# Performance work log

Hardware: AMD Instinct MI355X
Metric: run time of the kernel (lower is better)

Reference implementation:

```python
import jax, jax.numpy as jnp
import numpy as np

ALPHA = 4.0          # init alpha
THRESH = 0.693       # validity threshold (~ln 2) from the torch code
K = 8                # instances per class (labels are grouped in blocks of K)
N = 2048
D = 512
NUM_CLASSES = N // K


def setup_inputs() -> dict:
    key = jax.random.key(0)
    inputs = jax.random.normal(key, (N, D), dtype=jnp.float32)
    # grouped labels: [0]*K, [1]*K, ... (required by the original masked_select/resize logic)
    targets = jnp.repeat(jnp.arange(NUM_CLASSES, dtype=jnp.int32), K)
    return {"inputs": inputs, "targets": targets}


def reference(inputs, targets):
    n = inputs.shape[0]
    # x = alpha * L2-normalize(inputs)
    x = ALPHA * inputs / jnp.linalg.norm(inputs, axis=1, keepdims=True)
    # squared euclidean distance matrix [n, n]
    sq = jnp.sum(x * x, axis=1, keepdims=True)
    dist = sq + sq.T - 2.0 * (x @ x.T)

    eye = jnp.eye(n, dtype=bool)
    same = targets[:, None] == targets[None, :]
    pos_mask = same & ~eye            # positives (excluding self)
    neg_mask = ~same                  # negatives

    m = K - 1                         # positives per row
    n_neg = n - K                     # negatives per row
    # stable argsort puts True (0 after ~) positions first, preserving row-major order
    pos_idx = jnp.argsort(~pos_mask, axis=1)[:, :m]
    neg_idx = jnp.argsort(~neg_mask, axis=1)[:, :n_neg]
    pos_dist = jnp.take_along_axis(dist, pos_idx, axis=1)   # [n, m]
    neg_dist = jnp.take_along_axis(dist, neg_idx, axis=1)   # [n, n_neg]

    # triplet_mat[i, j, k] = log(exp(pos[i,k] - neg[i,j]) + 1)
    trip = jnp.log1p(jnp.exp(pos_dist[:, None, :] - neg_dist[:, :, None]))  # [n, n_neg, m]
    valid = trip > THRESH
    cnt = jnp.sum(valid, axis=(1, 2))                        # valid triplets per row
    row_sum = jnp.sum(jnp.where(valid, trip, 0.0), axis=(1, 2))
    row_mean = jnp.where(cnt > 0, row_sum / jnp.maximum(cnt, 1), 0.0)
    total = jnp.sum(cnt)
    loss = jnp.where(total > 0, jnp.sum(row_mean) / total, 0.0)

    accuracy = jnp.mean((cnt == 0).astype(jnp.float32))
    pos_d = jnp.mean(pos_dist)
    neg_d = jnp.mean(neg_dist)
    return loss, accuracy, pos_d, neg_d
```

## Files before the change

### kernel.cpp

```cpp
#include <hip/hip_runtime.h>
#include <hip/hip_bf16.h>
#include <math.h>

#define N 2048
#define D 512
#define KC 8
#define M (KC - 1)
#define NNEG (N - KC)
#define ALPHA 4.0f
#define THRESH 0.693f
#define LN2F 0.6931471805599453f
#define INV_LN2F 1.4426950408889634f
#define C2 (THRESH * INV_LN2F)

typedef unsigned short ushort_t;
using frag_ab = __attribute__((ext_vector_type(8))) short;
using frag_cd = __attribute__((ext_vector_type(4))) float;

__device__ __forceinline__ void gload16(const ushort_t* g, ushort_t* l) {
    __builtin_amdgcn_global_load_lds((const __attribute__((address_space(1))) unsigned int*)g,
                                     (__attribute__((address_space(3))) unsigned int*)l, 16, 0, 0);
}

__global__ __launch_bounds__(128) void normalize_kernel(const float* __restrict__ in,
                                                        ushort_t* __restrict__ xb,
                                                        float* __restrict__ sq) {
    int row = blockIdx.x;
    int tid = threadIdx.x;
    const float* r = in + (size_t)row * D;
    float p = 0.f;
    for (int d = tid; d < D; d += 128) { float v = r[d]; p += v * v; }
    __shared__ float red[128];
    red[tid] = p; __syncthreads();
    for (int s = 64; s > 0; s >>= 1) { if (tid < s) red[tid] += red[tid + s]; __syncthreads(); }
    float scale = ALPHA / sqrtf(red[0]);
    __syncthreads();
    float q = 0.f;
    for (int d = tid; d < D; d += 128) {
        float v = r[d] * scale;
        q += v * v;
        __hip_bfloat16 h = __float2bfloat16(v);
        xb[(size_t)row * D + d] = *(ushort_t*)&h;
    }
    red[tid] = q; __syncthreads();
    for (int s = 64; s > 0; s >>= 1) { if (tid < s) red[tid] += red[tid + s]; __syncthreads(); }
    if (tid == 0) sq[row] = red[0];
}

#define TM 64
#define TN 64
#define TK 64
#define NT (D / TK)

__global__ __launch_bounds__(256) void gemm_dist_mfma(const ushort_t* __restrict__ xb,
                                                      const float* __restrict__ sq,
                                                      float* __restrict__ dist) {
    __shared__ ushort_t As[2 * TM * TK];
    __shared__ ushort_t Bs[2 * TN * TK];
    int tid  = threadIdx.x;
    int lane = tid & 63;
    int w    = tid >> 6;
    int wm   = w >> 1, wn = w & 1;
    int quad = lane >> 4, l16 = lane & 15;
    int bi = blockIdx.y, bj = blockIdx.x;

    frag_cd acc[2][2];
    #pragma unroll
    for (int i = 0; i < 2; ++i)
        #pragma unroll
        for (int j = 0; j < 2; ++j)
            acc[i][j] = (frag_cd){0.f, 0.f, 0.f, 0.f};

    int c0 = tid, c1 = tid + 256;
    int r0 = c0 >> 3, sl0 = c0 & 7;
    int r1 = c1 >> 3, sl1 = c1 & 7;
    int g0 = (sl0 ^ (r0 & 7)) * 8;
    int g1 = (sl1 ^ (r1 & 7)) * 8;
    const ushort_t* gA0 = xb + (size_t)(bi * TM + r0) * D + g0;
    const ushort_t* gA1 = xb + (size_t)(bi * TM + r1) * D + g1;
    const ushort_t* gB0 = xb + (size_t)(bj * TN + r0) * D + g0;
    const ushort_t* gB1 = xb + (size_t)(bj * TN + r1) * D + g1;
    ushort_t* lA0 = As + c0 * 8;
    ushort_t* lA1 = As + c1 * 8;
    ushort_t* lB0 = Bs + c0 * 8;
    ushort_t* lB1 = Bs + c1 * 8;

    int xm = l16 & 7;
    int aoff[2][2], boff[2][2];
    #pragma unroll
    for (int i = 0; i < 2; ++i)
        #pragma unroll
        for (int kk = 0; kk < 2; ++kk) {
            aoff[i][kk] = (wm * 32 + i * 16 + l16) * TK + ((kk * 4 + quad) ^ xm) * 8;
            boff[i][kk] = (wn * 32 + i * 16 + l16) * TK + ((kk * 4 + quad) ^ xm) * 8;
        }

    gload16(gA0, lA0); gload16(gA1, lA1); gload16(gB0, lB0); gload16(gB1, lB1);
    int cur = 0;
    for (int t = 0; t < NT; ++t) {
        __syncthreads();
        if (t + 1 < NT) {
            int k0 = (t + 1) * TK;
            int bo = (cur ^ 1) * (TM * TK);
            gload16(gA0 + k0, lA0 + bo);
            gload16(gA1 + k0, lA1 + bo);
            gload16(gB0 + k0, lB0 + bo);
            gload16(gB1 + k0, lB1 + bo);
        }
        const ushort_t* Ab = As + cur * (TM * TK);
        const ushort_t* Bb = Bs + cur * (TN * TK);
        frag_ab a[2][2], b[2][2];
        #pragma unroll
        for (int i = 0; i < 2; ++i)
            #pragma unroll
            for (int kk = 0; kk < 2; ++kk) {
                a[i][kk] = *(const frag_ab*)(Ab + aoff[i][kk]);
                b[i][kk] = *(const frag_ab*)(Bb + boff[i][kk]);
            }
        #pragma unroll
        for (int kk = 0; kk < 2; ++kk)
            #pragma unroll
            for (int i = 0; i < 2; ++i)
                #pragma unroll
                for (int j = 0; j < 2; ++j)
                    acc[i][j] = __builtin_amdgcn_mfma_f32_16x16x32_bf16(a[i][kk], b[j][kk], acc[i][j], 0, 0, 0);
        cur ^= 1;
    }

    int row_base = bi * TM + wm * 32 + quad * 4;
    int col_base = bj * TN + wn * 32 + l16;
    #pragma unroll
    for (int j = 0; j < 2; ++j) {
        int col = col_base + j * 16;
        float sjv = sq[col];
        #pragma unroll
        for (int i = 0; i < 2; ++i) {
            int row = row_base + i * 16;
            #pragma unroll
            for (int r = 0; r < 4; ++r) {
                dist[(size_t)(row + r) * N + col] = sq[row + r] + sjv - 2.f * acc[i][j][r];
            }
        }
    }
}

__global__ __launch_bounds__(256) void triplet_kernel(const float* __restrict__ dist,
                                                      float4* __restrict__ rowres) {
    int i = blockIdx.x;
    int tid = threadIdx.x;
    int cs = (i >> 3) << 3;
    const float* drow = dist + (size_t)i * N;

    __shared__ float pos[M];
    if (tid == 0) {
        int c = 0;
        for (int j = cs; j < cs + KC; ++j)
            if (j != i) pos[c++] = drow[j];
    }
    __syncthreads();
    float p[M], ep[M];
    #pragma unroll
    for (int k = 0; k < M; ++k) { p[k] = pos[k]; ep[k] = __expf(p[k]); }

    float s2 = 0.f, nsum = 0.f;
    unsigned cnt = 0;
    for (int j = tid; j < N; j += 256) {
        if (j >= cs && j < cs + KC) continue;
        float neg = drow[j];
        nsum += neg;
        float en = __expf(-neg);
        #pragma unroll
        for (int k = 0; k < M; ++k) {
            float e = ep[k] * en;
            float l = __log2f(1.f + e);
            if (l > C2) { cnt++; s2 += l; }
        }
    }

    __shared__ float rs[256];
    __shared__ float rn[256];
    __shared__ unsigned rc[256];
    rs[tid] = s2; rn[tid] = nsum; rc[tid] = cnt;
    __syncthreads();
    for (int st = 128; st > 0; st >>= 1) {
        if (tid < st) { rs[tid] += rs[tid + st]; rn[tid] += rn[tid + st]; rc[tid] += rc[tid + st]; }
        __syncthreads();
    }
    if (tid == 0) {
        float psum = 0.f;
        #pragma unroll
        for (int k = 0; k < M; ++k) psum += p[k];
        rowres[i] = make_float4(rs[0], (float)rc[0], psum, rn[0]);
    }
}

__global__ __launch_bounds__(256) void final_reduce_kernel(const float4* __restrict__ rowres,
                                                           float* __restrict__ out) {
    int tid = threadIdx.x;
    double srm = 0.0, ps = 0.0, ns = 0.0;
    unsigned long long tot = 0; unsigned zr = 0;
    for (int i = tid; i < N; i += 256) {
        float4 r = rowres[i];
        unsigned c = (unsigned)r.y;
        if (c > 0) {
            float row_mean = r.x * LN2F / (float)c;
            srm += (double)row_mean;
            tot += c;
        } else {
            zr++;
        }
        ps += (double)r.z;
        ns += (double)r.w;
    }
    __shared__ double d0[256], d1[256], d2[256];
    __shared__ unsigned long long dt[256];
    __shared__ unsigned dz[256];
    d0[tid] = srm; d1[tid] = ps; d2[tid] = ns; dt[tid] = tot; dz[tid] = zr;
    __syncthreads();
    for (int st = 128; st > 0; st >>= 1) {
        if (tid < st) {
            d0[tid] += d0[tid + st]; d1[tid] += d1[tid + st]; d2[tid] += d2[tid + st];
            dt[tid] += dt[tid + st]; dz[tid] += dz[tid + st];
        }
        __syncthreads();
    }
    if (tid == 0) {
        unsigned long long total = dt[0];
        out[0] = (total > 0) ? (float)(d0[0] / (double)total) : 0.f;
        out[1] = (float)((double)dz[0] / (double)N);
        out[2] = (float)(d1[0] / (double)((size_t)N * M));
        out[3] = (float)(d2[0] / (double)((size_t)N * NNEG));
    }
}

extern "C" void kernel_launch(void* const* d_in, const int* in_sizes, int n_in,
                              void* d_out, int out_size, void* d_ws, size_t ws_size,
                              hipStream_t stream) {
    const float* inputs = (const float*)d_in[0];
    float* out = (float*)d_out;
    char* ws = (char*)d_ws;

    const size_t off_xb   = 0;
    const size_t off_sq   = off_xb + (size_t)N * D * sizeof(ushort_t);
    const size_t off_dist = off_sq + (size_t)N * sizeof(float) + 4096;
    const size_t off_row  = off_dist + (size_t)N * N * sizeof(float);
    const size_t needed   = off_row + (size_t)N * sizeof(float4);
    if (ws_size < needed) return;

    ushort_t* xb     = (ushort_t*)(ws + off_xb);
    float*    sq     = (float*)(ws + off_sq);
    float*    dist   = (float*)(ws + off_dist);
    float4*   rowres = (float4*)(ws + off_row);

    normalize_kernel<<<N, 128, 0, stream>>>(inputs, xb, sq);
    gemm_dist_mfma<<<dim3(N / TN, N / TM), 256, 0, stream>>>(xb, sq, dist);
    triplet_kernel<<<N, 256, 0, stream>>>(dist, rowres);
    final_reduce_kernel<<<1, 256, 0, stream>>>(rowres, out);
}
```

Baseline: 90.33 us.

## Fuse final reduction into triplet kernel and vectorize negative loads

Merges the single-block final reduction into the triplet kernel using a last-block-done atomic counter, which the GEMM kernel resets, saving one kernel launch. Each thread of the triplet kernel now loads 8 contiguous distances as two float4 values, and the thread that would load its own class block skips work entirely instead of branching per element. This adds an atomic and threadfence per block, and the tail reduction runs serially in the last block.

```diff
diff --git a/kernel.cpp b/kernel.cpp
--- a/kernel.cpp
+++ b/kernel.cpp
@@ -12,6 +12,7 @@
 #define LN2F 0.6931471805599453f
 #define INV_LN2F 1.4426950408889634f
 #define C2 (THRESH * INV_LN2F)
+
 
 typedef unsigned short ushort_t;
 using frag_ab = __attribute__((ext_vector_type(8))) short;
@@ -54,7 +55,8 @@
 
 __global__ __launch_bounds__(256) void gemm_dist_mfma(const ushort_t* __restrict__ xb,
                                                       const float* __restrict__ sq,
-                                                      float* __restrict__ dist) {
+                                                      float* __restrict__ dist,
+                                                      unsigned* __restrict__ counter) {
     __shared__ ushort_t As[2 * TM * TK];
     __shared__ ushort_t Bs[2 * TN * TK];
     int tid  = threadIdx.x;
@@ -63,6 +65,8 @@
     int wm   = w >> 1, wn = w & 1;
     int quad = lane >> 4, l16 = lane & 15;
     int bi = blockIdx.y, bj = blockIdx.x;
+
+    if (bi == 0 && bj == 0 && tid == 0) *counter = 0;
 
     frag_cd acc[2][2];
     #pragma unroll
@@ -144,8 +148,10 @@
     }
 }
 
-__global__ __launch_bounds__(256) void triplet_kernel(const float* __restrict__ dist,
-                                                      float4* __restrict__ rowres) {
+__global__ __launch_bounds__(256) void triplet_final_kernel(const float* __restrict__ dist,
+                                                            float4* __restrict__ rowres,
+                                                            unsigned* __restrict__ counter,
+                                                            float* __restrict__ out) {
     int i = blockIdx.x;
     int tid = threadIdx.x;
     int cs = (i >> 3) << 3;
@@ -164,16 +170,21 @@
 
     float s2 = 0.f, nsum = 0.f;
     unsigned cnt = 0;
-    for (int j = tid; j < N; j += 256) {
-        if (j >= cs && j < cs + KC) continue;
-        float neg = drow[j];
-        nsum += neg;
-        float en = __expf(-neg);
-        #pragma unroll
-        for (int k = 0; k < M; ++k) {
-            float e = ep[k] * en;
-            float l = __log2f(1.f + e);
-            if (l > C2) { cnt++; s2 += l; }
+    if (tid != (i >> 3)) {
+        const float4* d4 = (const float4*)(drow + tid * 8);
+        float4 v0 = d4[0], v1 = d4[1];
+        float neg8[8] = {v0.x, v0.y, v0.z, v0.w, v1.x, v1.y, v1.z, v1.w};
+        #pragma unroll
+        for (int e = 0; e < 8; ++e) {
+            float neg = neg8[e];
+            nsum += neg;
+            float en = __expf(-neg);
+            #pragma unroll
+            for (int k = 0; k < M; ++k) {
+                float ev = ep[k] * en;
+                float l = __log2f(1.f + ev);
+                if (l > C2) { cnt++; s2 += l; }
+            }
         }
     }
 
@@ -186,31 +197,34 @@
         if (tid < st) { rs[tid] += rs[tid + st]; rn[tid] += rn[tid + st]; rc[tid] += rc[tid + st]; }
         __syncthreads();
     }
+    __shared__ unsigned isLast;
     if (tid == 0) {
         float psum = 0.f;
         #pragma unroll
         for (int k = 0; k < M; ++k) psum += p[k];
         rowres[i] = make_float4(rs[0], (float)rc[0], psum, rn[0]);
-    }
-}
-
-__global__ __launch_bounds__(256) void final_reduce_kernel(const float4* __restrict__ rowres,
-                                                           float* __restrict__ out) {
-    int tid = threadIdx.x;
+        __threadfence();
+        unsigned old = atomicAdd(counter, 1u);
+        isLast = (old == N - 1) ? 1u : 0u;
+    }
+    __syncthreads();
+    if (isLast == 0) return;
+
+    __threadfence();
     double srm = 0.0, ps = 0.0, ns = 0.0;
     unsigned long long tot = 0; unsigned zr = 0;
-    for (int i = tid; i < N; i += 256) {
-        float4 r = rowres[i];
-        unsigned c = (unsigned)r.y;
+    for (int r = tid; r < N; r += 256) {
+        float4 v = rowres[r];
+        unsigned c = (unsigned)v.y;
         if (c > 0) {
-            float row_mean = r.x * LN2F / (float)c;
+            float row_mean = v.x * LN2F / (float)c;
             srm += (double)row_mean;
             tot += c;
         } else {
             zr++;
         }
-        ps += (double)r.z;
-        ns += (double)r.w;
+        ps += (double)v.z;
+        ns += (double)v.w;
     }
     __shared__ double d0[256], d1[256], d2[256];
     __shared__ unsigned long long dt[256];
@@ -244,16 +258,17 @@
     const size_t off_sq   = off_xb + (size_t)N * D * sizeof(ushort_t);
     const size_t off_dist = off_sq + (size_t)N * sizeof(float) + 4096;
     const size_t off_row  = off_dist + (size_t)N * N * sizeof(float);
-    const size_t needed   = off_row + (size_t)N * sizeof(float4);
+    const size_t off_cnt  = off_row + (size_t)N * sizeof(float4);
+    const size_t needed   = off_cnt + 64;
     if (ws_size < needed) return;
 
-    ushort_t* xb     = (ushort_t*)(ws + off_xb);
-    float*    sq     = (float*)(ws + off_sq);
-    float*    dist   = (float*)(ws + off_dist);
-    float4*   rowres = (float4*)(ws + off_row);
+    ushort_t* xb      = (ushort_t*)(ws + off_xb);
+    float*    sq      = (float*)(ws + off_sq);
+    float*    dist    = (float*)(ws + off_dist);
+    float4*   rowres  = (float4*)(ws + off_row);
+    unsigned* counter = (unsigned*)(ws + off_cnt);
 
     normalize_kernel<<<N, 128, 0, stream>>>(inputs, xb, sq);
-    gemm_dist_mfma<<<dim3(N / TN, N / TM), 256, 0, stream>>>(xb, sq, dist);
-    triplet_kernel<<<N, 256, 0, stream>>>(dist, rowres);
-    final_reduce_kernel<<<1, 256, 0, stream>>>(rowres, out);
-}
+    gemm_dist_mfma<<<dim3(N / TN, N / TM), 256, 0, stream>>>(xb, sq, dist, counter);
+    triplet_final_kernel<<<N, 256, 0, stream>>>(dist, rowres, counter, out);
+}
```

Measured after the change: 122.6 us. +35.7%, slower.
